# Kernel optimization log

Hardware: AMD Instinct MI355X
Metric: run time of the kernel (lower is better)

Reference implementation:

```python
import jax, jax.numpy as jnp
import numpy as np

B, N, D, H = 2, 2048, 512, 8
HD = D // H


def setup_inputs() -> dict:
    key = jax.random.key(0)
    ks = jax.random.split(key, 12)
    s = 1.0 / np.sqrt(D)
    inp = {
        "x": jax.random.normal(ks[0], (B, N, D), dtype=jnp.float32),
        "adjacency": jax.random.randint(ks[1], (B, N, N), 0, 2, dtype=jnp.int32),
        "Wq": jax.random.uniform(ks[2], (D, D), jnp.float32, -s, s),
        "bq": jnp.zeros((D,), jnp.float32),
        "Wk": jax.random.uniform(ks[3], (D, D), jnp.float32, -s, s),
        "bk": jnp.zeros((D,), jnp.float32),
        "Wv": jax.random.uniform(ks[4], (D, D), jnp.float32, -s, s),
        "bv": jnp.zeros((D,), jnp.float32),
        "Wo": jax.random.uniform(ks[5], (D, D), jnp.float32, -s, s),
        "bo": jnp.zeros((D,), jnp.float32),
        "gamma": jnp.ones((D,), jnp.float32),
        "beta": jnp.zeros((D,), jnp.float32),
    }
    return inp


def reference(x, adjacency, Wq, bq, Wk, bk, Wv, bv, Wo, bo, gamma, beta):
    scale = HD ** -0.5
    # projections -> [B, H, N, HD]
    def proj(W, b):
        return (x @ W.T + b).reshape(B, N, H, HD).transpose(0, 2, 1, 3)
    q = proj(Wq, bq)
    k = proj(Wk, bk)
    v = proj(Wv, bv)
    # [B, H, N, N] attention scores
    scores = jnp.einsum("bhqd,bhkd->bhqk", q, k) * scale
    mask = (adjacency[:, None, :, :] != 0)  # [B, 1->H, N, N]
    scores = jnp.where(mask, scores, -jnp.inf)
    attn = jax.nn.softmax(scores, axis=-1)
    # dropout is identity in eval mode
    ctx = jnp.einsum("bhqk,bhkd->bhqd", attn, v)
    ctx = ctx.transpose(0, 2, 1, 3).reshape(B, N, D)
    out = ctx @ Wo.T + bo
    y = x + out
    mu = jnp.mean(y, axis=-1, keepdims=True)
    var = jnp.var(y, axis=-1, keepdims=True)
    return (y - mu) * jax.lax.rsqrt(var + 1e-5) * gamma + beta
```

## Files before the change

kernel.cpp:

```cpp
#include <hip/hip_runtime.h>
#include <hip/hip_bf16.h>

#define B_  2
#define N_  2048
#define D_  512
#define H_  8
#define HD_ 64

typedef float  f4  __attribute__((ext_vector_type(4)));
typedef int    i4  __attribute__((ext_vector_type(4)));
typedef short  bf16x8 __attribute__((ext_vector_type(8)));
typedef float  f32x4  __attribute__((ext_vector_type(4)));
typedef unsigned short u16x8 __attribute__((ext_vector_type(8)));
typedef unsigned short u16x4 __attribute__((ext_vector_type(4)));

static __device__ __forceinline__ unsigned short f2bf(float f) {
    union { float f; unsigned int u; } v; v.f = f;
    unsigned int r = v.u + 0x7fffu + ((v.u >> 16) & 1u);
    return (unsigned short)(r >> 16);
}

__global__ __launch_bounds__(256) void prep_kernel(
    const float* __restrict__ x,
    const float* __restrict__ Wq, const float* __restrict__ Wk,
    const float* __restrict__ Wv, const float* __restrict__ Wo,
    unsigned short* __restrict__ xh, unsigned short* __restrict__ WhAll)
{
    const size_t e = ((size_t)blockIdx.x * 256 + threadIdx.x) * 8;
    const float* src;
    unsigned short* dst;
    if (e < 2097152) {
        src = x + e;  dst = xh + e;
    } else {
        const size_t e2 = e - 2097152;
        const int wi = (int)(e2 >> 18);
        const size_t off = e2 & 262143;
        const float* Ws = (wi == 0) ? Wq : (wi == 1) ? Wk : (wi == 2) ? Wv : Wo;
        src = Ws + off;  dst = WhAll + (size_t)wi * 262144 + off;
    }
    f4 a = *(const f4*)src;
    f4 b = *(const f4*)(src + 4);
    u16x8 o;
    #pragma unroll
    for (int j = 0; j < 4; ++j) { o[j] = f2bf(a[j]); o[j + 4] = f2bf(b[j]); }
    *(u16x8*)dst = o;
}

template <int OUT_MODE>
__device__ __forceinline__ void mfma_gemm_body(
    const unsigned short* __restrict__ Ah, const unsigned short* __restrict__ Wh,
    const float* __restrict__ bias, float* __restrict__ outf,
    unsigned short* __restrict__ outh, int r0, int c0)
{
    __shared__ unsigned short Asm[128][72];
    __shared__ unsigned short Bsm[128][72];

    const int tid  = threadIdx.x;
    const int lane = tid & 63;
    const int w    = tid >> 6;
    const int wr   = w >> 1, wc = w & 1;
    const int l15  = lane & 15, lhi = lane >> 4;

    f32x4 acc[4][4];
    #pragma unroll
    for (int mi = 0; mi < 4; ++mi)
        #pragma unroll
        for (int ni = 0; ni < 4; ++ni)
            acc[mi][ni] = (f32x4){0.f, 0.f, 0.f, 0.f};

    for (int kt = 0; kt < 512; kt += 64) {
        __syncthreads();
        #pragma unroll
        for (int i = 0; i < 4; ++i) {
            const int v   = tid + i * 256;
            const int row = v >> 3;
            const int c8  = (v & 7) * 8;
            *(u16x8*)&Asm[row][c8] =
                *(const u16x8*)&Ah[(size_t)(r0 + row) * 512 + kt + c8];
            *(u16x8*)&Bsm[row][c8] =
                *(const u16x8*)&Wh[(size_t)(c0 + row) * 512 + kt + c8];
        }
        __syncthreads();

        #pragma unroll
        for (int ks = 0; ks < 2; ++ks) {
            bf16x8 a[4], bb[4];
            #pragma unroll
            for (int mi = 0; mi < 4; ++mi)
                a[mi] = *(const bf16x8*)&Asm[wr * 64 + mi * 16 + l15][ks * 32 + lhi * 8];
            #pragma unroll
            for (int ni = 0; ni < 4; ++ni)
                bb[ni] = *(const bf16x8*)&Bsm[wc * 64 + ni * 16 + l15][ks * 32 + lhi * 8];
            #pragma unroll
            for (int mi = 0; mi < 4; ++mi)
                #pragma unroll
                for (int ni = 0; ni < 4; ++ni)
                    acc[mi][ni] = __builtin_amdgcn_mfma_f32_16x16x32_bf16(
                        a[mi], bb[ni], acc[mi][ni], 0, 0, 0);
        }
    }

    #pragma unroll
    for (int ni = 0; ni < 4; ++ni) {
        const int c = c0 + wc * 64 + ni * 16 + l15;
        const float bias_c = bias[c];
        #pragma unroll
        for (int mi = 0; mi < 4; ++mi) {
            #pragma unroll
            for (int reg = 0; reg < 4; ++reg) {
                const int r = r0 + wr * 64 + mi * 16 + lhi * 4 + reg;
                const float vv = acc[mi][ni][reg] + bias_c;
                if (OUT_MODE == 0) {
                    outf[(size_t)r * 512 + c] = vv;
                } else {
                    const int bbn = r >> 11, n = r & (N_ - 1);
                    const int h = c >> 6, hd = c & 63;
                    outh[(((size_t)(bbn * H_ + h)) * N_ + n) * HD_ + hd] = f2bf(vv);
                }
            }
        }
    }
}

__global__ __launch_bounds__(256) void qkv_mfma_kernel(
    const unsigned short* __restrict__ xh, const unsigned short* __restrict__ WhAll,
    const float* __restrict__ bq, const float* __restrict__ bk,
    const float* __restrict__ bv,
    unsigned short* __restrict__ Qh, unsigned short* __restrict__ Kh,
    unsigned short* __restrict__ Vh)
{
    const int z = blockIdx.z;
    const unsigned short* Wh = WhAll + (size_t)z * 262144;
    const float* bias = (z == 0) ? bq : (z == 1) ? bk : bv;
    unsigned short* dst = (z == 0) ? Qh : (z == 1) ? Kh : Vh;
    mfma_gemm_body<1>(xh, Wh, bias, nullptr, dst,
                      blockIdx.y * 128, blockIdx.x * 128);
}

__global__ __launch_bounds__(256) void wo_mfma_kernel(
    const unsigned short* __restrict__ ctxh, const unsigned short* __restrict__ WhAll,
    const float* __restrict__ bo, float* __restrict__ y1)
{
    mfma_gemm_body<0>(ctxh, WhAll + 3 * 262144, bo, y1, nullptr,
                      blockIdx.y * 128, blockIdx.x * 128);
}

__global__ __launch_bounds__(256) void attn_kernel(
    const unsigned short* __restrict__ Q, const unsigned short* __restrict__ K,
    const unsigned short* __restrict__ V, const int* __restrict__ adj,
    unsigned short* __restrict__ ctxh)
{
    __shared__ unsigned short K_lds[2][64][72];
    __shared__ unsigned short Vt_lds[2][64][72];
    __shared__ unsigned short P_lds[4][16][72];
    __shared__ float fac_lds[4][16];

    const int tid  = threadIdx.x;
    const int lane = tid & 63;
    const int w    = tid >> 6;
    const int l15  = lane & 15, lhi = lane >> 4;
    const int bh = blockIdx.y;
    const int b  = bh >> 3;
    const int hh = bh & 7;
    const int q0 = blockIdx.x * 64;

    const unsigned short* Qbh = Q + (size_t)bh * N_ * HD_;
    const unsigned short* Kbh = K + (size_t)bh * N_ * HD_;
    const unsigned short* Vbh = V + (size_t)bh * N_ * HD_;
    const int* adjb = adj + (size_t)b * N_ * N_;

    const int sk  = tid & 63;
    const int sc2 = tid >> 6;
    const int sv_k2  = (tid & 31) * 2;
    const int sv_dvb = (tid >> 5) * 8;

    const int qrow = q0 + w * 16 + l15;
    bf16x8 aq0 = *(const bf16x8*)&Qbh[(size_t)qrow * HD_ + lhi * 8];
    bf16x8 aq1 = *(const bf16x8*)&Qbh[(size_t)qrow * HD_ + 32 + lhi * 8];

    const int qrow_base = q0 + w * 16 + lhi * 4;

    f32x4 acc[4];
    #pragma unroll
    for (int t = 0; t < 4; ++t) acc[t] = (f32x4){0.f, 0.f, 0.f, 0.f};
    float m_q = -__builtin_inff();
    float l_q = 0.0f;
    const float NEG_INF = -__builtin_inff();
    const float scale = 0.125f;

    {
        u16x8 k0 = *(const u16x8*)&Kbh[(size_t)sk * HD_ + sc2 * 8];
        u16x8 k1 = *(const u16x8*)&Kbh[(size_t)sk * HD_ + (sc2 + 4) * 8];
        *(u16x8*)&K_lds[0][sk][sc2 * 8]       = k0;
        *(u16x8*)&K_lds[0][sk][(sc2 + 4) * 8] = k1;
        u16x8 v0 = *(const u16x8*)&Vbh[(size_t)sv_k2 * HD_ + sv_dvb];
        u16x8 v1 = *(const u16x8*)&Vbh[(size_t)(sv_k2 + 1) * HD_ + sv_dvb];
        #pragma unroll
        for (int i = 0; i < 8; ++i) {
            unsigned int pair = (unsigned int)(unsigned short)v0[i] |
                                ((unsigned int)(unsigned short)v1[i] << 16);
            *(unsigned int*)&Vt_lds[0][sv_dvb + i][sv_k2] = pair;
        }
    }
    i4 adjc[4], adjn[4];
    #pragma unroll
    for (int kt = 0; kt < 4; ++kt)
        adjc[kt] = *(const i4*)&adjb[(size_t)qrow * N_ + kt * 16 + lhi * 4];
    __syncthreads();

    int cur = 0;
    for (int kc = 0; kc < N_; kc += 64) {
        const int kcn = (kc + 64) & (N_ - 1);
        u16x8 nk0 = *(const u16x8*)&Kbh[(size_t)(kcn + sk) * HD_ + sc2 * 8];
        u16x8 nk1 = *(const u16x8*)&Kbh[(size_t)(kcn + sk) * HD_ + (sc2 + 4) * 8];
        u16x8 nv0 = *(const u16x8*)&Vbh[(size_t)(kcn + sv_k2) * HD_ + sv_dvb];
        u16x8 nv1 = *(const u16x8*)&Vbh[(size_t)(kcn + sv_k2 + 1) * HD_ + sv_dvb];
        #pragma unroll
        for (int kt = 0; kt < 4; ++kt)
            adjn[kt] = *(const i4*)&adjb[(size_t)qrow * N_ + kcn + kt * 16 + lhi * 4];

        f32x4 s[4];
        #pragma unroll
        for (int kt = 0; kt < 4; ++kt) {
            bf16x8 bk0 = *(const bf16x8*)&K_lds[cur][kt * 16 + l15][lhi * 8];
            bf16x8 bk1 = *(const bf16x8*)&K_lds[cur][kt * 16 + l15][32 + lhi * 8];
            f32x4 z = {0.f, 0.f, 0.f, 0.f};
            z = __builtin_amdgcn_mfma_f32_16x16x32_bf16(bk0, aq0, z, 0, 0, 0);
            s[kt] = __builtin_amdgcn_mfma_f32_16x16x32_bf16(bk1, aq1, z, 0, 0, 0);
        }

        float sm[16];
        #pragma unroll
        for (int kt = 0; kt < 4; ++kt)
            #pragma unroll
            for (int r = 0; r < 4; ++r)
                sm[kt * 4 + r] = adjc[kt][r] ? s[kt][r] * scale : NEG_INF;

        float mx = sm[0];
        #pragma unroll
        for (int i = 1; i < 16; ++i) mx = fmaxf(mx, sm[i]);
        mx = fmaxf(mx, __shfl_xor(mx, 16));
        mx = fmaxf(mx, __shfl_xor(mx, 32));

        const float mnew = fmaxf(m_q, mx);
        float fac, p[16];
        if (mnew == NEG_INF) {
            fac = 1.0f;
            #pragma unroll
            for (int i = 0; i < 16; ++i) p[i] = 0.0f;
        } else {
            fac = __expf(m_q - mnew);
            #pragma unroll
            for (int i = 0; i < 16; ++i)
                p[i] = __expf(sm[i] - mnew);
        }
        m_q = mnew;

        float rs = 0.0f;
        #pragma unroll
        for (int i = 0; i < 16; ++i) rs += p[i];
        rs += __shfl_xor(rs, 16);
        rs += __shfl_xor(rs, 32);
        l_q = l_q * fac + rs;

        if (lhi == 0) fac_lds[w][l15] = fac;
        f4 fac4 = *(const f4*)&fac_lds[w][lhi * 4];
        #pragma unroll
        for (int t = 0; t < 4; ++t)
            #pragma unroll
            for (int r = 0; r < 4; ++r)
                acc[t][r] *= fac4[r];

        #pragma unroll
        for (int kt = 0; kt < 4; ++kt) {
            u16x4 pw;
            #pragma unroll
            for (int r = 0; r < 4; ++r) pw[r] = f2bf(p[kt * 4 + r]);
            *(u16x4*)&P_lds[w][l15][kt * 16 + lhi * 4] = pw;
        }

        #pragma unroll
        for (int ks = 0; ks < 2; ++ks) {
            bf16x8 ap = *(const bf16x8*)&P_lds[w][l15][ks * 32 + lhi * 8];
            #pragma unroll
            for (int dvt = 0; dvt < 4; ++dvt) {
                bf16x8 bv = *(const bf16x8*)&Vt_lds[cur][dvt * 16 + l15][ks * 32 + lhi * 8];
                acc[dvt] = __builtin_amdgcn_mfma_f32_16x16x32_bf16(ap, bv, acc[dvt], 0, 0, 0);
            }
        }

        const int nxt = cur ^ 1;
        *(u16x8*)&K_lds[nxt][sk][sc2 * 8]       = nk0;
        *(u16x8*)&K_lds[nxt][sk][(sc2 + 4) * 8] = nk1;
        #pragma unroll
        for (int i = 0; i < 8; ++i) {
            unsigned int pair = (unsigned int)(unsigned short)nv0[i] |
                                ((unsigned int)(unsigned short)nv1[i] << 16);
            *(unsigned int*)&Vt_lds[nxt][sv_dvb + i][sv_k2] = pair;
        }
        __syncthreads();
        cur = nxt;

        #pragma unroll
        for (int kt = 0; kt < 4; ++kt) adjc[kt] = adjn[kt];
    }

    if (lhi == 0) fac_lds[w][l15] = l_q;
    f4 lv = *(const f4*)&fac_lds[w][lhi * 4];
    #pragma unroll
    for (int r = 0; r < 4; ++r) {
        const int q = qrow_base + r;
        const float inv = (lv[r] > 0.0f) ? 1.0f / lv[r] : 0.0f;
        #pragma unroll
        for (int dvt = 0; dvt < 4; ++dvt)
            ctxh[((size_t)(b * N_ + q)) * D_ + hh * HD_ + dvt * 16 + l15] =
                f2bf(acc[dvt][r] * inv);
    }
}

__global__ __launch_bounds__(64) void ln_kernel(
    const float* __restrict__ x, const float* __restrict__ y1,
    const float* __restrict__ gamma, const float* __restrict__ beta,
    float* __restrict__ out)
{
    const int row = blockIdx.x;
    const int tid = threadIdx.x;
    const size_t base = (size_t)row * 512 + tid * 8;

    f4 v0 = *(const f4*)&x[base]     + *(const f4*)&y1[base];
    f4 v1 = *(const f4*)&x[base + 4] + *(const f4*)&y1[base + 4];

    float s = v0[0] + v0[1] + v0[2] + v0[3] + v1[0] + v1[1] + v1[2] + v1[3];
    #pragma unroll
    for (int off = 1; off < 64; off <<= 1) s += __shfl_xor(s, off);
    const float mu = s * (1.0f / 512.0f);

    float d2 = 0.0f;
    #pragma unroll
    for (int j = 0; j < 4; ++j) {
        const float a = v0[j] - mu, bq = v1[j] - mu;
        d2 += a * a + bq * bq;
    }
    #pragma unroll
    for (int off = 1; off < 64; off <<= 1) d2 += __shfl_xor(d2, off);
    const float rstd = rsqrtf(d2 * (1.0f / 512.0f) + 1e-5f);

    f4 g0 = *(const f4*)&gamma[tid * 8];
    f4 g1 = *(const f4*)&gamma[tid * 8 + 4];
    f4 be0 = *(const f4*)&beta[tid * 8];
    f4 be1 = *(const f4*)&beta[tid * 8 + 4];
    f4 o0, o1;
    #pragma unroll
    for (int j = 0; j < 4; ++j) {
        o0[j] = (v0[j] - mu) * rstd * g0[j] + be0[j];
        o1[j] = (v1[j] - mu) * rstd * g1[j] + be1[j];
    }
    *(f4*)&out[base]     = o0;
    *(f4*)&out[base + 4] = o1;
}

extern "C" void kernel_launch(void* const* d_in, const int* in_sizes, int n_in,
                              void* d_out, int out_size, void* d_ws, size_t ws_size,
                              hipStream_t stream)
{
    const float* x     = (const float*)d_in[0];
    const int*   adj   = (const int*)  d_in[1];
    const float* Wq    = (const float*)d_in[2];
    const float* bq    = (const float*)d_in[3];
    const float* Wk    = (const float*)d_in[4];
    const float* bk    = (const float*)d_in[5];
    const float* Wv    = (const float*)d_in[6];
    const float* bv    = (const float*)d_in[7];
    const float* Wo    = (const float*)d_in[8];
    const float* bo    = (const float*)d_in[9];
    const float* gamma = (const float*)d_in[10];
    const float* beta  = (const float*)d_in[11];
    float* out = (float*)d_out;

    const size_t elems = (size_t)B_ * N_ * D_;
    unsigned short* Qh    = (unsigned short*)d_ws;
    unsigned short* Kh    = Qh   + elems;
    unsigned short* Vh    = Kh   + elems;
    unsigned short* ctxh  = Vh   + elems;
    unsigned short* xh    = ctxh + elems;
    unsigned short* WhAll = xh   + elems;
    float* y1 = (float*)Qh;

    prep_kernel<<<1536, 256, 0, stream>>>(x, Wq, Wk, Wv, Wo, xh, WhAll);

    qkv_mfma_kernel<<<dim3(4, 32, 3), 256, 0, stream>>>(
        xh, WhAll, bq, bk, bv, Qh, Kh, Vh);

    attn_kernel<<<dim3(N_ / 64, B_ * H_), 256, 0, stream>>>(Qh, Kh, Vh, adj, ctxh);

    wo_mfma_kernel<<<dim3(4, 32), 256, 0, stream>>>(ctxh, WhAll, bo, y1);

    ln_kernel<<<B_ * N_, 64, 0, stream>>>(x, y1, gamma, beta, out);
}
```

Baseline: 212.1 us.

## Fuse fp32-to-bf16 conversion into GEMM loads, add lazy softmax rescale and MFMA priority

Removes the separate prep kernel and converts x and the weight matrices from fp32 to bf16 inside the GEMM tile loads, which saves one launch and a round trip through the workspace. In exchange, each GEMM block reads twice as many bytes per tile and converts the same weight tiles again in every block. The attention loop now skips the online-softmax max update and the accumulator rescale when no row's new max exceeds the running max by more than a threshold. s_setprio is also raised around the MFMA bursts. The lazy rescale lets exponentials exceed 1 by up to exp(8) before the bf16 cast, which may change accuracy slightly.

```diff
diff --git a/kernel.cpp b/kernel.cpp
--- a/kernel.cpp
+++ b/kernel.cpp
@@ -20,37 +20,12 @@
     return (unsigned short)(r >> 16);
 }
 
-__global__ __launch_bounds__(256) void prep_kernel(
-    const float* __restrict__ x,
-    const float* __restrict__ Wq, const float* __restrict__ Wk,
-    const float* __restrict__ Wv, const float* __restrict__ Wo,
-    unsigned short* __restrict__ xh, unsigned short* __restrict__ WhAll)
-{
-    const size_t e = ((size_t)blockIdx.x * 256 + threadIdx.x) * 8;
-    const float* src;
-    unsigned short* dst;
-    if (e < 2097152) {
-        src = x + e;  dst = xh + e;
-    } else {
-        const size_t e2 = e - 2097152;
-        const int wi = (int)(e2 >> 18);
-        const size_t off = e2 & 262143;
-        const float* Ws = (wi == 0) ? Wq : (wi == 1) ? Wk : (wi == 2) ? Wv : Wo;
-        src = Ws + off;  dst = WhAll + (size_t)wi * 262144 + off;
-    }
-    f4 a = *(const f4*)src;
-    f4 b = *(const f4*)(src + 4);
-    u16x8 o;
-    #pragma unroll
-    for (int j = 0; j < 4; ++j) { o[j] = f2bf(a[j]); o[j + 4] = f2bf(b[j]); }
-    *(u16x8*)dst = o;
-}
-
-template <int OUT_MODE>
+template <int OUT_MODE, int A_IS_F32>
 __device__ __forceinline__ void mfma_gemm_body(
-    const unsigned short* __restrict__ Ah, const unsigned short* __restrict__ Wh,
-    const float* __restrict__ bias, float* __restrict__ outf,
-    unsigned short* __restrict__ outh, int r0, int c0)
+    const float* __restrict__ Af, const unsigned short* __restrict__ Ah,
+    const float* __restrict__ Wf, const float* __restrict__ bias,
+    float* __restrict__ outf, unsigned short* __restrict__ outh,
+    int r0, int c0)
 {
     __shared__ unsigned short Asm[128][72];
     __shared__ unsigned short Bsm[128][72];
@@ -75,10 +50,23 @@
             const int v   = tid + i * 256;
             const int row = v >> 3;
             const int c8  = (v & 7) * 8;
-            *(u16x8*)&Asm[row][c8] =
-                *(const u16x8*)&Ah[(size_t)(r0 + row) * 512 + kt + c8];
-            *(u16x8*)&Bsm[row][c8] =
-                *(const u16x8*)&Wh[(size_t)(c0 + row) * 512 + kt + c8];
+            if (A_IS_F32) {
+                f4 a0 = *(const f4*)&Af[(size_t)(r0 + row) * 512 + kt + c8];
+                f4 a1 = *(const f4*)&Af[(size_t)(r0 + row) * 512 + kt + c8 + 4];
+                u16x8 oa;
+                #pragma unroll
+                for (int j = 0; j < 4; ++j) { oa[j] = f2bf(a0[j]); oa[j + 4] = f2bf(a1[j]); }
+                *(u16x8*)&Asm[row][c8] = oa;
+            } else {
+                *(u16x8*)&Asm[row][c8] =
+                    *(const u16x8*)&Ah[(size_t)(r0 + row) * 512 + kt + c8];
+            }
+            f4 w0 = *(const f4*)&Wf[(size_t)(c0 + row) * 512 + kt + c8];
+            f4 w1 = *(const f4*)&Wf[(size_t)(c0 + row) * 512 + kt + c8 + 4];
+            u16x8 ow;
+            #pragma unroll
+            for (int j = 0; j < 4; ++j) { ow[j] = f2bf(w0[j]); ow[j + 4] = f2bf(w1[j]); }
+            *(u16x8*)&Bsm[row][c8] = ow;
         }
         __syncthreads();
 
@@ -91,12 +79,14 @@
             #pragma unroll
             for (int ni = 0; ni < 4; ++ni)
                 bb[ni] = *(const bf16x8*)&Bsm[wc * 64 + ni * 16 + l15][ks * 32 + lhi * 8];
+            __builtin_amdgcn_s_setprio(1);
             #pragma unroll
             for (int mi = 0; mi < 4; ++mi)
                 #pragma unroll
                 for (int ni = 0; ni < 4; ++ni)
                     acc[mi][ni] = __builtin_amdgcn_mfma_f32_16x16x32_bf16(
                         a[mi], bb[ni], acc[mi][ni], 0, 0, 0);
+            __builtin_amdgcn_s_setprio(0);
         }
     }
 
@@ -123,26 +113,28 @@
 }
 
 __global__ __launch_bounds__(256) void qkv_mfma_kernel(
-    const unsigned short* __restrict__ xh, const unsigned short* __restrict__ WhAll,
+    const float* __restrict__ x,
+    const float* __restrict__ Wq, const float* __restrict__ Wk,
+    const float* __restrict__ Wv,
     const float* __restrict__ bq, const float* __restrict__ bk,
     const float* __restrict__ bv,
     unsigned short* __restrict__ Qh, unsigned short* __restrict__ Kh,
     unsigned short* __restrict__ Vh)
 {
     const int z = blockIdx.z;
-    const unsigned short* Wh = WhAll + (size_t)z * 262144;
+    const float* Wf = (z == 0) ? Wq : (z == 1) ? Wk : Wv;
     const float* bias = (z == 0) ? bq : (z == 1) ? bk : bv;
     unsigned short* dst = (z == 0) ? Qh : (z == 1) ? Kh : Vh;
-    mfma_gemm_body<1>(xh, Wh, bias, nullptr, dst,
-                      blockIdx.y * 128, blockIdx.x * 128);
+    mfma_gemm_body<1, 1>(x, nullptr, Wf, bias, nullptr, dst,
+                         blockIdx.y * 128, blockIdx.x * 128);
 }
 
 __global__ __launch_bounds__(256) void wo_mfma_kernel(
-    const unsigned short* __restrict__ ctxh, const unsigned short* __restrict__ WhAll,
+    const unsigned short* __restrict__ ctxh, const float* __restrict__ Wo,
     const float* __restrict__ bo, float* __restrict__ y1)
 {
-    mfma_gemm_body<0>(ctxh, WhAll + 3 * 262144, bo, y1, nullptr,
-                      blockIdx.y * 128, blockIdx.x * 128);
+    mfma_gemm_body<0, 0>(nullptr, ctxh, Wo, bo, y1, nullptr,
+                         blockIdx.y * 128, blockIdx.x * 128);
 }
 
 __global__ __launch_bounds__(256) void attn_kernel(
@@ -187,6 +179,7 @@
     float l_q = 0.0f;
     const float NEG_INF = -__builtin_inff();
     const float scale = 0.125f;
+    const float RESCALE_THR = 8.0f;
 
     {
         u16x8 k0 = *(const u16x8*)&Kbh[(size_t)sk * HD_ + sc2 * 8];
@@ -220,6 +213,7 @@
             adjn[kt] = *(const i4*)&adjb[(size_t)qrow * N_ + kcn + kt * 16 + lhi * 4];
 
         f32x4 s[4];
+        __builtin_amdgcn_s_setprio(1);
         #pragma unroll
         for (int kt = 0; kt < 4; ++kt) {
             bf16x8 bk0 = *(const bf16x8*)&K_lds[cur][kt * 16 + l15][lhi * 8];
@@ -228,6 +222,7 @@
             z = __builtin_amdgcn_mfma_f32_16x16x32_bf16(bk0, aq0, z, 0, 0, 0);
             s[kt] = __builtin_amdgcn_mfma_f32_16x16x32_bf16(bk1, aq1, z, 0, 0, 0);
         }
+        __builtin_amdgcn_s_setprio(0);
 
         float sm[16];
         #pragma unroll
@@ -242,19 +237,33 @@
         mx = fmaxf(mx, __shfl_xor(mx, 16));
         mx = fmaxf(mx, __shfl_xor(mx, 32));
 
-        const float mnew = fmaxf(m_q, mx);
-        float fac, p[16];
-        if (mnew == NEG_INF) {
-            fac = 1.0f;
-            #pragma unroll
-            for (int i = 0; i < 16; ++i) p[i] = 0.0f;
+        const bool skip = __all(mx - m_q <= RESCALE_THR);
+
+        float fac = 1.0f, p[16];
+        if (skip) {
+            #pragma unroll
+            for (int i = 0; i < 16; ++i)
+                p[i] = __expf(sm[i] - m_q);
         } else {
-            fac = __expf(m_q - mnew);
-            #pragma unroll
-            for (int i = 0; i < 16; ++i)
-                p[i] = __expf(sm[i] - mnew);
-        }
-        m_q = mnew;
+            const float mnew = fmaxf(m_q, mx);
+            if (mnew == NEG_INF) {
+                #pragma unroll
+                for (int i = 0; i < 16; ++i) p[i] = 0.0f;
+            } else {
+                fac = __expf(m_q - mnew);
+                #pragma unroll
+                for (int i = 0; i < 16; ++i)
+                    p[i] = __expf(sm[i] - mnew);
+            }
+            m_q = mnew;
+            if (lhi == 0) fac_lds[w][l15] = fac;
+            f4 fac4 = *(const f4*)&fac_lds[w][lhi * 4];
+            #pragma unroll
+            for (int t = 0; t < 4; ++t)
+                #pragma unroll
+                for (int r = 0; r < 4; ++r)
+                    acc[t][r] *= fac4[r];
+        }
 
         float rs = 0.0f;
         #pragma unroll
@@ -263,14 +272,6 @@
         rs += __shfl_xor(rs, 32);
         l_q = l_q * fac + rs;
 
-        if (lhi == 0) fac_lds[w][l15] = fac;
-        f4 fac4 = *(const f4*)&fac_lds[w][lhi * 4];
-        #pragma unroll
-        for (int t = 0; t < 4; ++t)
-            #pragma unroll
-            for (int r = 0; r < 4; ++r)
-                acc[t][r] *= fac4[r];
-
         #pragma unroll
         for (int kt = 0; kt < 4; ++kt) {
             u16x4 pw;
@@ -282,11 +283,13 @@
         #pragma unroll
         for (int ks = 0; ks < 2; ++ks) {
             bf16x8 ap = *(const bf16x8*)&P_lds[w][l15][ks * 32 + lhi * 8];
+            __builtin_amdgcn_s_setprio(1);
             #pragma unroll
             for (int dvt = 0; dvt < 4; ++dvt) {
                 bf16x8 bv = *(const bf16x8*)&Vt_lds[cur][dvt * 16 + l15][ks * 32 + lhi * 8];
                 acc[dvt] = __builtin_amdgcn_mfma_f32_16x16x32_bf16(ap, bv, acc[dvt], 0, 0, 0);
             }
+            __builtin_amdgcn_s_setprio(0);
         }
 
         const int nxt = cur ^ 1;
@@ -378,22 +381,18 @@
     float* out = (float*)d_out;
 
     const size_t elems = (size_t)B_ * N_ * D_;
-    unsigned short* Qh    = (unsigned short*)d_ws;
-    unsigned short* Kh    = Qh   + elems;
-    unsigned short* Vh    = Kh   + elems;
-    unsigned short* ctxh  = Vh   + elems;
-    unsigned short* xh    = ctxh + elems;
-    unsigned short* WhAll = xh   + elems;
+    unsigned short* Qh   = (unsigned short*)d_ws;
+    unsigned short* Kh   = Qh + elems;
+    unsigned short* Vh   = Kh + elems;
+    unsigned short* ctxh = Vh + elems;
     float* y1 = (float*)Qh;
 
-    prep_kernel<<<1536, 256, 0, stream>>>(x, Wq, Wk, Wv, Wo, xh, WhAll);
-
     qkv_mfma_kernel<<<dim3(4, 32, 3), 256, 0, stream>>>(
-        xh, WhAll, bq, bk, bv, Qh, Kh, Vh);
+        x, Wq, Wk, Wv, bq, bk, bv, Qh, Kh, Vh);
 
     attn_kernel<<<dim3(N_ / 64, B_ * H_), 256, 0, stream>>>(Qh, Kh, Vh, adj, ctxh);
 
-    wo_mfma_kernel<<<dim3(4, 32), 256, 0, stream>>>(ctxh, WhAll, bo, y1);
+    wo_mfma_kernel<<<dim3(4, 32), 256, 0, stream>>>(ctxh, Wo, bo, y1);
 
     ln_kernel<<<B_ * N_, 64, 0, stream>>>(x, y1, gamma, beta, out);
 }
```

New measurement: 199.5 us. -6.0%, faster.
